# Optimization experiments

Measured on AMD Instinct MI355X. Metric: run time of the kernel, lower is better.

The kernel has to match this reference:

```python
import jax, jax.numpy as jnp
import numpy as np

D_MODEL, D_K, D_V, H = 1024, 128, 128, 8


def setup_inputs() -> dict:
    key = jax.random.key(0)
    ks = jax.random.split(key, 14)
    B, NQ, NK = 8, 1024, 1024
    def lin(kw, out_d, in_d):
        # xavier_uniform weight, zero bias
        lim = jnp.sqrt(6.0 / (in_d + out_d))
        return jax.random.uniform(kw, (out_d, in_d), jnp.float32, -lim, lim)
    return {
        "queries": jax.random.normal(ks[0], (B, NQ, D_MODEL), jnp.float32),
        "keys": jax.random.normal(ks[1], (B, NK, D_MODEL), jnp.float32),
        "values": jax.random.normal(ks[2], (B, NK, D_MODEL), jnp.float32),
        "language_signals": jax.random.normal(ks[3], (B, NQ, D_MODEL), jnp.float32),
        "Wq": lin(ks[4], H * D_K, D_MODEL), "bq": jnp.zeros((H * D_K,), jnp.float32),
        "Wk": lin(ks[5], H * D_K, D_MODEL), "bk": jnp.zeros((H * D_K,), jnp.float32),
        "Wv": lin(ks[6], H * D_V, D_MODEL), "bv": jnp.zeros((H * D_V,), jnp.float32),
        "Ws": lin(ks[7], H * D_K, D_MODEL), "bs": jnp.zeros((H * D_K,), jnp.float32),
        "Wo": lin(ks[8], D_MODEL, H * D_V), "bo": jnp.zeros((D_MODEL,), jnp.float32),
    }


def reference(queries, keys, values, language_signals,
              Wq, bq, Wk, bk, Wv, bv, Ws, bs, Wo, bo):
    b, nq, _ = queries.shape
    nk = keys.shape[1]
    scale = 1.0 / jnp.sqrt(jnp.asarray(D_K, queries.dtype))
    # project and split heads -> (b, h, n, d)
    q = (queries @ Wq.T + bq).reshape(b, nq, H, D_K).transpose(0, 2, 1, 3)
    s = (language_signals @ Ws.T + bs).reshape(b, nq, H, D_K).transpose(0, 2, 1, 3)
    k = (keys @ Wk.T + bk).reshape(b, nk, H, D_K).transpose(0, 2, 1, 3)
    v = (values @ Wv.T + bv).reshape(b, nk, H, D_V).transpose(0, 2, 1, 3)
    attn = jnp.einsum('bhqd,bhkd->bhqk', q, k) * scale           # (b,h,nq,nk)
    lang = jnp.einsum('bhqd,bhqd->bhq', q, s) * scale            # diagonal sentinel score
    combined = jnp.concatenate([attn, lang[..., None]], axis=-1)  # (b,h,nq,nk+1)
    p = jax.nn.softmax(combined, axis=-1)
    # per-query value set is [v; s_i]: split matmul into kv part + sentinel part
    out = jnp.einsum('bhqk,bhkd->bhqd', p[..., :nk], v) + p[..., nk:] * s
    out = out.transpose(0, 2, 1, 3).reshape(b, nq, H * D_V)
    return out @ Wo.T + bo
```

## Files before the change

kernel.cpp:

```cpp
#include <hip/hip_runtime.h>
#include <hip/hip_bf16.h>


typedef __attribute__((ext_vector_type(8))) short s16x8;
typedef __attribute__((ext_vector_type(4))) float f32x4;
typedef __attribute__((ext_vector_type(16))) float f32x16;
typedef __attribute__((ext_vector_type(4))) unsigned int u32x4;

#define DEVI static __device__ __forceinline__

constexpr int BATCH = 8;
constexpr int SEQ   = 1024;
constexpr int NH    = 8;
constexpr int DH    = 128;
constexpr int DM    = 1024;

DEVI short bf16r(float f) {
  __hip_bfloat16 h = __float2bfloat16(f);
  return *reinterpret_cast<short*>(&h);
}
DEVI float bf2f(short s) {
  __hip_bfloat16 h;
  *reinterpret_cast<short*>(&h) = s;
  return __bfloat162float(h);
}
DEVI s16x8 cvt8(const float4& a, const float4& b) {
  s16x8 r;
  r[0] = bf16r(a.x); r[1] = bf16r(a.y); r[2] = bf16r(a.z); r[3] = bf16r(a.w);
  r[4] = bf16r(b.x); r[5] = bf16r(b.y); r[6] = bf16r(b.z); r[7] = bf16r(b.w);
  return r;
}
DEVI unsigned int pack2bf(float a, float b) {
  return (unsigned int)(unsigned short)bf16r(a) |
         ((unsigned int)(unsigned short)bf16r(b) << 16);
}

#define GLOAD16(g, l)                                                        \
  __builtin_amdgcn_global_load_lds(                                          \
      (const __attribute__((address_space(1))) unsigned int*)(g),            \
      (__attribute__((address_space(3))) unsigned int*)(l), 16, 0, 0)

DEVI f32x4 mfma(s16x8 a, s16x8 b, f32x4 c) {
  return __builtin_amdgcn_mfma_f32_16x16x32_bf16(a, b, c, 0, 0, 0);
}
DEVI f32x16 mfma32(s16x8 a, s16x8 b, f32x16 c) {
  return __builtin_amdgcn_mfma_f32_32x32x16_bf16(a, b, c, 0, 0, 0);
}

__global__ __launch_bounds__(256)
void cvt_all(const float* __restrict__ a0, const float* __restrict__ a1,
             const float* __restrict__ a2, const float* __restrict__ a3,
             const float* __restrict__ w0, const float* __restrict__ w1,
             const float* __restrict__ w2, const float* __restrict__ w3,
             const float* __restrict__ w4,
             short* __restrict__ d0, short* __restrict__ d1,
             short* __restrict__ d2, short* __restrict__ d3,
             short* __restrict__ e0, short* __restrict__ e1,
             short* __restrict__ e2, short* __restrict__ e3,
             short* __restrict__ e4) {
  const float* s; short* d; int idx;
  int bid = blockIdx.x;
  if (bid < 16384) {
    int which = bid >> 12; idx = bid & 4095;
    switch (which) {
      case 0: s = a0; d = d0; break;
      case 1: s = a1; d = d1; break;
      case 2: s = a2; d = d2; break;
      default: s = a3; d = d3; break;
    }
  } else {
    int r = bid - 16384;
    int which = r >> 9; idx = r & 511;
    switch (which) {
      case 0: s = w0; d = e0; break;
      case 1: s = w1; d = e1; break;
      case 2: s = w2; d = e2; break;
      case 3: s = w3; d = e3; break;
      default: s = w4; d = e4; break;
    }
  }
  size_t i = ((size_t)idx * 256 + threadIdx.x) * 8;
  float4 a = *(const float4*)(s + i);
  float4 b = *(const float4*)(s + i + 4);
  *(s16x8*)(d + i) = cvt8(a, b);
}

DEVI void gemm_core(const short* __restrict__ A, const short* __restrict__ W,
                    short* Alds, short* Blds, int m0, int n0,
                    f32x4 (&acc)[4][4]) {
  const int tid = threadIdx.x, lane = tid & 63, wid = tid >> 6;
  const int wm = wid >> 1, wn = wid & 1, lr = lane & 15, lg = lane >> 4;
  const int srow = wid * 32 + (lane >> 3);
  const int scb  = (lane & 7) * 16;

  for (int k0 = 0; k0 < DM; k0 += 64) {
    if (k0) __syncthreads();
#pragma unroll
    for (int t = 0; t < 4; t++) {
      int row = srow + t * 8;
      int cbs = scb ^ ((row & 7) << 4);
      GLOAD16((const char*)A + ((size_t)(m0 + row) * DM + k0) * 2 + cbs,
              (char*)Alds + wid * 4096 + t * 1024);
      GLOAD16((const char*)W + ((size_t)(n0 + row) * DM + k0) * 2 + cbs,
              (char*)Blds + wid * 4096 + t * 1024);
    }
    __syncthreads();
#pragma unroll
    for (int kk = 0; kk < 2; kk++) {
      s16x8 af[4], bf[4];
#pragma unroll
      for (int i = 0; i < 4; i++) {
        int row = wm * 64 + i * 16 + lr;
        af[i] = *(const s16x8*)((const char*)Alds + row * 128 +
                                ((kk * 64 + lg * 16) ^ ((row & 7) << 4)));
      }
#pragma unroll
      for (int j = 0; j < 4; j++) {
        int row = wn * 64 + j * 16 + lr;
        bf[j] = *(const s16x8*)((const char*)Blds + row * 128 +
                                ((kk * 64 + lg * 16) ^ ((row & 7) << 4)));
      }
#pragma unroll
      for (int i = 0; i < 4; i++)
#pragma unroll
        for (int j = 0; j < 4; j++)
          acc[i][j] = mfma(af[i], bf[j], acc[i][j]);
    }
  }
}

__global__ __launch_bounds__(256)
void proj_gemm(const short* __restrict__ qa, const short* __restrict__ ka,
               const short* __restrict__ va, const short* __restrict__ sa,
               const short* __restrict__ wq, const short* __restrict__ wk,
               const short* __restrict__ wv, const short* __restrict__ wsn,
               const float* __restrict__ bq, const float* __restrict__ bk,
               const float* __restrict__ bv, const float* __restrict__ bsn,
               short* __restrict__ Qo, short* __restrict__ Ko,
               short* __restrict__ Vo, short* __restrict__ So) {
  __shared__ short Alds[128 * 64];
  __shared__ short Blds[128 * 64];
  const int z = blockIdx.z;
  const short* A; const short* W; const float* bias; short* C;
  switch (z) {
    case 0: A = qa; W = wq;  bias = bq;  C = Qo; break;
    case 1: A = ka; W = wk;  bias = bk;  C = Ko; break;
    case 2: A = va; W = wv;  bias = bv;  C = Vo; break;
    default: A = sa; W = wsn; bias = bsn; C = So; break;
  }
  const int m0 = blockIdx.x * 128, n0 = blockIdx.y * 128;
  f32x4 acc[4][4] = {};
  gemm_core(A, W, Alds, Blds, m0, n0, acc);

  const int lane = threadIdx.x & 63, wid = threadIdx.x >> 6;
  const int wm = wid >> 1, wn = wid & 1, lr = lane & 15, lg = lane >> 4;
#pragma unroll
  for (int i = 0; i < 4; i++) {
#pragma unroll
    for (int r = 0; r < 4; r++) {
      int m = m0 + wm * 64 + i * 16 + lg * 4 + r;
      int bb = m >> 10, sq = m & 1023;
#pragma unroll
      for (int j = 0; j < 4; j++) {
        int n = n0 + wn * 64 + j * 16 + lr;
        float v = acc[i][j][r] + bias[n];
        int hh = n >> 7, d = n & 127;
        if (z == 2)
          C[((size_t)(bb * NH + hh) * DH + d) * SEQ + sq] = bf16r(v);
        else
          C[((size_t)(bb * NH + hh) * SEQ + sq) * DH + d] = bf16r(v);
      }
    }
  }
}

__global__ __launch_bounds__(256)
void out_gemm(const short* __restrict__ A, const short* __restrict__ W,
              const float* __restrict__ bias, float* __restrict__ C) {
  __shared__ short Alds[128 * 64];
  __shared__ short Blds[128 * 64];
  const int bid = blockIdx.x;
  const int wg = (bid & 7) * 64 + (bid >> 3);
  const int m0 = (wg >> 3) * 128, n0 = (wg & 7) * 128;
  f32x4 acc[4][4] = {};
  gemm_core(A, W, Alds, Blds, m0, n0, acc);

  const int lane = threadIdx.x & 63, wid = threadIdx.x >> 6;
  const int wm = wid >> 1, wn = wid & 1, lr = lane & 15, lg = lane >> 4;
#pragma unroll
  for (int i = 0; i < 4; i++)
#pragma unroll
    for (int r = 0; r < 4; r++) {
      int m = m0 + wm * 64 + i * 16 + lg * 4 + r;
#pragma unroll
      for (int j = 0; j < 4; j++) {
        int n = n0 + wn * 64 + j * 16 + lr;
        C[(size_t)m * DM + n] = acc[i][j][r] + bias[n];
      }
    }
}

DEVI void stage_kv(const char* Kg, const char* Vg, int k0n,
                   short* Kd, short* Vd, int tid, int wave) {
  const int krow_l = tid >> 4, kslot = tid & 15;
  const int vrow_l = tid >> 3, vslot = tid & 7;
#pragma unroll
  for (int ln = 0; ln < 2; ln++) {
    int kr = ln * 32 + krow_l;
    int ss = kslot ^ (((kr & 7) << 1) ^ ((kr >> 3) & 3));
    GLOAD16(Kg + (size_t)(k0n + kr) * 256 + ss * 16,
            (char*)Kd + ln * 8192 + wave * 1024);
  }
#pragma unroll
  for (int ln = 0; ln < 2; ln++) {
    int dr = ln * 64 + vrow_l;
    int ss = vslot ^ ((dr & 7) ^ ((dr >> 3) & 3));
    GLOAD16(Vg + (size_t)dr * 2048 + (size_t)k0n * 2 + ss * 16,
            (char*)Vd + ln * 8192 + wave * 1024);
  }
}

__global__ __launch_bounds__(512, 2)
void attn_kernel(const short* __restrict__ Qb, const short* __restrict__ Kb,
                 const short* __restrict__ Vtb, const short* __restrict__ Sb,
                 short* __restrict__ att) {
  __shared__ short Klds[2][64 * 128];
  __shared__ short Vtlds[2][128 * 64];

  const int tid = threadIdx.x, lane = tid & 63, wave = tid >> 6;
  const int l31 = lane & 31, hi = lane >> 5;
  const int bid = blockIdx.x;
  const int logical = (bid & 7) * 32 + (bid >> 3);
  const int hb = logical >> 2, qt = logical & 3;
  const int b = hb >> 3, h = hb & 7;
  const int q0 = qt * 256 + wave * 32;
  const size_t base = (size_t)(b * NH + h) * SEQ * DH;
  const char* Kg = (const char*)(Kb + base);
  const char* Vg = (const char*)(Vtb + base);
  const float scale = 0.08838834764831845f * 1.44269504088896340f;

  s16x8 qf[8];
  {
    const char* qrow = (const char*)(Qb + base) + (size_t)(q0 + l31) * 256 + hi * 16;
#pragma unroll
    for (int kd = 0; kd < 8; kd++) qf[kd] = *(const s16x8*)(qrow + kd * 32);
  }

  float m_run = -INFINITY, l_run = 0.f;
  f32x16 oacc[4] = {};

  const int v4r = ((((lane & 7) << 1) ^ ((lane >> 3) & 3))) << 4;
  const int v3r = (((lane & 7) ^ ((lane >> 3) & 3))) << 4;

  stage_kv(Kg, Vg, 0, Klds[0], Vtlds[0], tid, wave);

  for (int it = 0; it < 16; ++it) {
    const int cur = it & 1;
    __syncthreads();
    if (it < 15)
      stage_kv(Kg, Vg, (it + 1) * 64, Klds[cur ^ 1], Vtlds[cur ^ 1], tid, wave);

    f32x16 st0 = {}, st1 = {};
    const char* Kb0 = (const char*)Klds[cur] + l31 * 256;
    __builtin_amdgcn_s_setprio(1);
#pragma unroll
    for (int kd = 0; kd < 8; kd++) {
      int co = (kd * 32 + hi * 16) ^ v4r;
      s16x8 a0 = *(const s16x8*)(Kb0 + co);
      s16x8 a1 = *(const s16x8*)(Kb0 + 32 * 256 + co);
      st0 = mfma32(a0, qf[kd], st0);
      st1 = mfma32(a1, qf[kd], st1);
    }
    __builtin_amdgcn_s_setprio(0);

    float traw = -INFINITY;
#pragma unroll
    for (int r = 0; r < 16; r++) {
      traw = fmaxf(traw, st0[r]);
      traw = fmaxf(traw, st1[r]);
    }
    traw = fmaxf(traw, __shfl_xor(traw, 32));
    float tmax = traw * scale;
    const bool skip = __all(tmax - m_run <= 8.f);
    float m_new = skip ? m_run : fmaxf(m_run, tmax);
    float psum = 0.f;
    unsigned W0[8], W1[8];
#pragma unroll
    for (int i = 0; i < 8; i++) {
      float p0 = exp2f(fmaf(st0[2 * i],     scale, -m_new));
      float p1 = exp2f(fmaf(st0[2 * i + 1], scale, -m_new));
      float p2 = exp2f(fmaf(st1[2 * i],     scale, -m_new));
      float p3 = exp2f(fmaf(st1[2 * i + 1], scale, -m_new));
      psum += (p0 + p1) + (p2 + p3);
      W0[i] = pack2bf(p0, p1);
      W1[i] = pack2bf(p2, p3);
    }
    psum += __shfl_xor(psum, 32);
    if (skip) {
      l_run += psum;
    } else {
      float fac = exp2f(m_run - m_new);
      l_run = l_run * fac + psum;
      m_run = m_new;
#pragma unroll
      for (int reg = 0; reg < 16; reg++) {
        int qs = (reg & 3) + 8 * (reg >> 2);
        float fr = __shfl(fac, qs + 4 * hi);
#pragma unroll
        for (int dt = 0; dt < 4; dt++) oacc[dt][reg] *= fr;
      }
    }

    s16x8 pa[4];
#pragma unroll
    for (int ks = 0; ks < 4; ks++) {
      const int s4 = (ks & 1) * 4;
      unsigned a0, a1, b0, b1;
      if (ks >> 1) { a0 = W1[s4]; a1 = W1[s4 + 1]; b0 = W1[s4 + 2]; b1 = W1[s4 + 3]; }
      else         { a0 = W0[s4]; a1 = W0[s4 + 1]; b0 = W0[s4 + 2]; b1 = W0[s4 + 3]; }
      unsigned snd0 = hi ? a0 : b0, snd1 = hi ? a1 : b1;
      unsigned rem0 = __shfl_xor(snd0, 32), rem1 = __shfl_xor(snd1, 32);
      unsigned w0 = hi ? rem0 : a0;
      unsigned w1 = hi ? rem1 : a1;
      unsigned w2 = hi ? b0 : rem0;
      unsigned w3 = hi ? b1 : rem1;
      u32x4 t4 = {w0, w1, w2, w3};
      pa[ks] = __builtin_bit_cast(s16x8, t4);
    }

    const char* Vb0 = (const char*)Vtlds[cur] + l31 * 128;
    __builtin_amdgcn_s_setprio(1);
#pragma unroll
    for (int dt = 0; dt < 4; dt++) {
#pragma unroll
      for (int ks = 0; ks < 4; ks++) {
        int co = (ks * 32 + hi * 16) ^ v3r;
        s16x8 bv = *(const s16x8*)(Vb0 + dt * 4096 + co);
        oacc[dt] = mfma32(pa[ks], bv, oacc[dt]);
      }
    }
    __builtin_amdgcn_s_setprio(0);
  }

  s16x8 sf[8];
  {
    const char* srow = (const char*)(Sb + base) + (size_t)(q0 + l31) * 256 + hi * 16;
#pragma unroll
    for (int kd = 0; kd < 8; kd++) sf[kd] = *(const s16x8*)(srow + kd * 32);
  }
  float dot = 0.f;
#pragma unroll
  for (int kd = 0; kd < 8; kd++)
#pragma unroll
    for (int j = 0; j < 8; j++) dot += bf2f(qf[kd][j]) * bf2f(sf[kd][j]);
  dot += __shfl_xor(dot, 32);
  float sc = dot * scale;
  float m_new = fmaxf(m_run, sc);
  float fac = exp2f(m_run - m_new);
  float ps = exp2f(sc - m_new);
  l_run = l_run * fac + ps;
  float inv_l = 1.f / l_run;

#pragma unroll
  for (int reg = 0; reg < 16; reg++) {
    int qs = (reg & 3) + 8 * (reg >> 2) + 4 * hi;
    int qsl = (reg & 3) + 8 * (reg >> 2);
    float fr = __shfl(fac,   qsl + 4 * hi);
    float pr = __shfl(ps,    qsl + 4 * hi);
    float il = __shfl(inv_l, qsl + 4 * hi);
    int qg = q0 + qs;
    const short* Sr = Sb + base + (size_t)qg * DH;
    short* orow = att + ((size_t)b * SEQ + qg) * (NH * DH) + h * DH;
#pragma unroll
    for (int dt = 0; dt < 4; dt++) {
      int d = dt * 32 + l31;
      float v = oacc[dt][reg] * fr + pr * bf2f(Sr[d]);
      orow[d] = bf16r(v * il);
    }
  }
}

extern "C" void kernel_launch(void* const* d_in, const int* in_sizes, int n_in,
                              void* d_out, int out_size, void* d_ws, size_t ws_size,
                              hipStream_t stream) {
  const float* queries = (const float*)d_in[0];
  const float* keys    = (const float*)d_in[1];
  const float* values  = (const float*)d_in[2];
  const float* lang    = (const float*)d_in[3];
  const float* Wq = (const float*)d_in[4];  const float* bq = (const float*)d_in[5];
  const float* Wk = (const float*)d_in[6];  const float* bk = (const float*)d_in[7];
  const float* Wv = (const float*)d_in[8];  const float* bv = (const float*)d_in[9];
  const float* Ws = (const float*)d_in[10]; const float* bs = (const float*)d_in[11];
  const float* Wo = (const float*)d_in[12]; const float* bo = (const float*)d_in[13];
  float* out = (float*)d_out;

  short* ws = (short*)d_ws;
  const size_t NE = (size_t)BATCH * SEQ * DM;
  const size_t WE = (size_t)DM * DM;
  short* qbf = ws;
  short* kbf = qbf + NE;
  short* vbf = kbf + NE;
  short* sbf = vbf + NE;
  short* Qb  = sbf + NE;
  short* Kb  = Qb  + NE;
  short* Vtb = Kb  + NE;
  short* Sb  = Vtb + NE;
  short* wqb = Sb  + NE;
  short* wkb = wqb + WE;
  short* wvb = wkb + WE;
  short* wsb = wvb + WE;
  short* wob = wsb + WE;
  short* att = qbf;

  hipLaunchKernelGGL(cvt_all, dim3(16384 + 2560), dim3(256), 0, stream,
                     queries, keys, values, lang, Wq, Wk, Wv, Ws, Wo,
                     qbf, kbf, vbf, sbf, wqb, wkb, wvb, wsb, wob);

  hipLaunchKernelGGL(proj_gemm, dim3(64, 8, 4), dim3(256), 0, stream,
                     qbf, kbf, vbf, sbf, wqb, wkb, wvb, wsb,
                     bq, bk, bv, bs, Qb, Kb, Vtb, Sb);

  hipLaunchKernelGGL(attn_kernel, dim3(256), dim3(512), 0, stream,
                     Qb, Kb, Vtb, Sb, att);

  hipLaunchKernelGGL(out_gemm, dim3(512), dim3(256), 0, stream,
                     att, wob, bo, out);
}
```

Baseline: 215.6 us.

## Rewrite projection GEMM with 256x256 tiles and double-buffered pipelined loads

Replaces the 128x128-tile projection GEMM with a 512-thread kernel computing 256x256 tiles. It double-buffers LDS and interleaves direct global-to-LDS loads with four MFMA phases per k-step, using barriers and setprio. A swizzled 1D grid is meant to improve L2 reuse. The larger tile cuts global traffic per FLOP and hides load latency, at the cost of heavy LDS use (128KB) and register pressure, plus fewer blocks (512) to fill the CUs.

After: 241.8 us. +12.2%, slower.

```diff
diff --git a/kernel.cpp b/kernel.cpp
--- a/kernel.cpp
+++ b/kernel.cpp
@@ -129,18 +129,27 @@
   }
 }
 
-__global__ __launch_bounds__(256)
-void proj_gemm(const short* __restrict__ qa, const short* __restrict__ ka,
-               const short* __restrict__ va, const short* __restrict__ sa,
-               const short* __restrict__ wq, const short* __restrict__ wk,
-               const short* __restrict__ wv, const short* __restrict__ wsn,
-               const float* __restrict__ bq, const float* __restrict__ bk,
-               const float* __restrict__ bv, const float* __restrict__ bsn,
-               short* __restrict__ Qo, short* __restrict__ Ko,
-               short* __restrict__ Vo, short* __restrict__ So) {
-  __shared__ short Alds[128 * 64];
-  __shared__ short Blds[128 * 64];
-  const int z = blockIdx.z;
+__global__ __launch_bounds__(512, 2)
+void proj_gemm256(const short* __restrict__ qa, const short* __restrict__ ka,
+                  const short* __restrict__ va, const short* __restrict__ sa,
+                  const short* __restrict__ wq, const short* __restrict__ wk,
+                  const short* __restrict__ wv, const short* __restrict__ wsn,
+                  const float* __restrict__ bq, const float* __restrict__ bk,
+                  const float* __restrict__ bv, const float* __restrict__ bsn,
+                  short* __restrict__ Qo, short* __restrict__ Ko,
+                  short* __restrict__ Vo, short* __restrict__ So) {
+  __shared__ short Alds[2][256 * 64];
+  __shared__ short Blds[2][256 * 64];
+
+  const int tid = threadIdx.x, lane = tid & 63, wid = tid >> 6;
+  const int wm = wid >> 2, wn = wid & 3, lr = lane & 15, lg = lane >> 4;
+
+  const int swz = (blockIdx.x & 7) * 64 + (blockIdx.x >> 3);
+  const int z = swz >> 7;
+  const int rem = swz & 127;
+  const int n0 = (rem >> 5) << 8;
+  const int m0 = (rem & 31) << 8;
+
   const short* A; const short* W; const float* bias; short* C;
   switch (z) {
     case 0: A = qa; W = wq;  bias = bq;  C = Qo; break;
@@ -148,22 +157,152 @@
     case 2: A = va; W = wv;  bias = bv;  C = Vo; break;
     default: A = sa; W = wsn; bias = bsn; C = So; break;
   }
-  const int m0 = blockIdx.x * 128, n0 = blockIdx.y * 128;
-  f32x4 acc[4][4] = {};
-  gemm_core(A, W, Alds, Blds, m0, n0, acc);
-
-  const int lane = threadIdx.x & 63, wid = threadIdx.x >> 6;
-  const int wm = wid >> 1, wn = wid & 1, lr = lane & 15, lg = lane >> 4;
-#pragma unroll
-  for (int i = 0; i < 4; i++) {
+  const char* Ag = (const char*)A + (size_t)m0 * 2048;
+  const char* Wg = (const char*)W + (size_t)n0 * 2048;
+
+  const int sR  = wid * 8 + (lane >> 3);
+  const int sCB = (((lane & 7) ^ (lane >> 3)) << 4);
+  const int lgb = lg * 16, rsw = (lr & 7) << 4;
+  const int ko0 = lgb ^ rsw, ko1 = (64 + lgb) ^ rsw;
+
+#define STG(Gb, r0, kb, Lb, off)                                             \
+  GLOAD16((Gb) + (size_t)((r0) + sR) * 2048 + (kb) + sCB,                    \
+          (char*)(Lb) + (off) + wid * 1024)
+
+  {
+    char* pa0 = (char*)Alds[0]; char* pb0 = (char*)Blds[0];
+    char* pa1 = (char*)Alds[1]; char* pb1 = (char*)Blds[1];
+    STG(Ag,   0, 0, pa0, 0);     STG(Ag, 128, 0, pa0, 16384);
+    STG(Ag,  64, 0, pa0, 8192);  STG(Ag, 192, 0, pa0, 24576);
+    STG(Wg,   0, 0, pb0, 0);     STG(Wg,  64, 0, pb0, 8192);
+    STG(Wg, 128, 0, pb0, 16384); STG(Wg, 192, 0, pb0, 24576);
+    STG(Ag,   0, 128, pa1, 0);     STG(Ag, 128, 128, pa1, 16384);
+    STG(Wg,   0, 128, pb1, 0);     STG(Wg,  64, 128, pb1, 8192);
+    STG(Ag,  64, 128, pa1, 8192);  STG(Ag, 192, 128, pa1, 24576);
+  }
+  asm volatile("s_waitcnt vmcnt(6)" ::: "memory");
+  __builtin_amdgcn_s_barrier();
+
+  f32x4 acc[8][4] = {};
+  const int rA0 = wm * 128 + lr;
+  const int rB0 = wn * 64 + lr;
+
+#pragma unroll 2
+  for (int kt = 0; kt < 16; ++kt) {
+    const char* Ab = (const char*)Alds[kt & 1];
+    const char* Bb = (const char*)Blds[kt & 1];
+    char* AbS = (char*)Alds[kt & 1];
+    char* BbS = (char*)Blds[kt & 1];
+    char* BbN = (char*)Blds[(kt + 1) & 1];
+    const int kb1 = (kt + 1) * 128, kb2 = (kt + 2) * 128;
+
+    s16x8 af[8], b0f[4], b1f[4];
+#pragma unroll
+    for (int mf = 0; mf < 4; mf++) {
+      int ro = (rA0 + mf * 16) * 128;
+      af[2 * mf]     = *(const s16x8*)(Ab + ro + ko0);
+      af[2 * mf + 1] = *(const s16x8*)(Ab + ro + ko1);
+    }
+#pragma unroll
+    for (int nf = 0; nf < 2; nf++) {
+      int ro = (rB0 + nf * 16) * 128;
+      b0f[2 * nf]     = *(const s16x8*)(Bb + ro + ko0);
+      b0f[2 * nf + 1] = *(const s16x8*)(Bb + ro + ko1);
+    }
+    if (kt + 1 < 16) {
+      STG(Wg, 128, kb1, BbN, 16384);
+      STG(Wg, 192, kb1, BbN, 24576);
+    }
+    asm volatile("s_waitcnt lgkmcnt(8)" ::: "memory");
+    __builtin_amdgcn_s_barrier();
+    asm volatile("s_waitcnt lgkmcnt(0)" ::: "memory");
+    __builtin_amdgcn_s_setprio(1);
+#pragma unroll
+    for (int mf = 0; mf < 4; mf++)
+#pragma unroll
+      for (int nf = 0; nf < 2; nf++) {
+        acc[mf][nf] = mfma(af[2 * mf],     b0f[2 * nf],     acc[mf][nf]);
+        acc[mf][nf] = mfma(af[2 * mf + 1], b0f[2 * nf + 1], acc[mf][nf]);
+      }
+    __builtin_amdgcn_s_setprio(0);
+    __builtin_amdgcn_s_barrier();
+
+#pragma unroll
+    for (int nf = 0; nf < 2; nf++) {
+      int ro = (rB0 + 32 + nf * 16) * 128;
+      b1f[2 * nf]     = *(const s16x8*)(Bb + ro + ko0);
+      b1f[2 * nf + 1] = *(const s16x8*)(Bb + ro + ko1);
+    }
+    if (kt + 2 < 16) {
+      STG(Ag,   0, kb2, AbS, 0);
+      STG(Ag, 128, kb2, AbS, 16384);
+    }
+    __builtin_amdgcn_s_barrier();
+    asm volatile("s_waitcnt lgkmcnt(0)" ::: "memory");
+    __builtin_amdgcn_s_setprio(1);
+#pragma unroll
+    for (int mf = 0; mf < 4; mf++)
+#pragma unroll
+      for (int nf = 0; nf < 2; nf++) {
+        acc[mf][nf + 2] = mfma(af[2 * mf],     b1f[2 * nf],     acc[mf][nf + 2]);
+        acc[mf][nf + 2] = mfma(af[2 * mf + 1], b1f[2 * nf + 1], acc[mf][nf + 2]);
+      }
+    __builtin_amdgcn_s_setprio(0);
+    __builtin_amdgcn_s_barrier();
+
+#pragma unroll
+    for (int mf = 0; mf < 4; mf++) {
+      int ro = (rA0 + 64 + mf * 16) * 128;
+      af[2 * mf]     = *(const s16x8*)(Ab + ro + ko0);
+      af[2 * mf + 1] = *(const s16x8*)(Ab + ro + ko1);
+    }
+    if (kt + 2 < 16) {
+      STG(Wg,  0, kb2, BbS, 0);
+      STG(Wg, 64, kb2, BbS, 8192);
+    }
+    __builtin_amdgcn_s_barrier();
+    asm volatile("s_waitcnt lgkmcnt(0)" ::: "memory");
+    __builtin_amdgcn_s_setprio(1);
+#pragma unroll
+    for (int mf = 0; mf < 4; mf++)
+#pragma unroll
+      for (int nf = 0; nf < 2; nf++) {
+        acc[mf + 4][nf + 2] = mfma(af[2 * mf],     b1f[2 * nf],     acc[mf + 4][nf + 2]);
+        acc[mf + 4][nf + 2] = mfma(af[2 * mf + 1], b1f[2 * nf + 1], acc[mf + 4][nf + 2]);
+      }
+    __builtin_amdgcn_s_setprio(0);
+    __builtin_amdgcn_s_barrier();
+
+    if (kt + 2 < 16) {
+      STG(Ag,  64, kb2, AbS, 8192);
+      STG(Ag, 192, kb2, AbS, 24576);
+    }
+    __builtin_amdgcn_s_barrier();
+    __builtin_amdgcn_s_setprio(1);
+#pragma unroll
+    for (int mf = 0; mf < 4; mf++)
+#pragma unroll
+      for (int nf = 0; nf < 2; nf++) {
+        acc[mf + 4][nf] = mfma(af[2 * mf],     b0f[2 * nf],     acc[mf + 4][nf]);
+        acc[mf + 4][nf] = mfma(af[2 * mf + 1], b0f[2 * nf + 1], acc[mf + 4][nf]);
+      }
+    __builtin_amdgcn_s_setprio(0);
+    if (kt < 14) asm volatile("s_waitcnt vmcnt(6)" ::: "memory");
+    else         asm volatile("s_waitcnt vmcnt(0)" ::: "memory");
+    __builtin_amdgcn_s_barrier();
+  }
+#undef STG
+
+#pragma unroll
+  for (int mf = 0; mf < 8; mf++) {
 #pragma unroll
     for (int r = 0; r < 4; r++) {
-      int m = m0 + wm * 64 + i * 16 + lg * 4 + r;
+      int m = m0 + wm * 128 + mf * 16 + lg * 4 + r;
       int bb = m >> 10, sq = m & 1023;
 #pragma unroll
-      for (int j = 0; j < 4; j++) {
-        int n = n0 + wn * 64 + j * 16 + lr;
-        float v = acc[i][j][r] + bias[n];
+      for (int nf = 0; nf < 4; nf++) {
+        int n = n0 + wn * 64 + nf * 16 + lr;
+        float v = acc[mf][nf][r] + bias[n];
         int hh = n >> 7, d = n & 127;
         if (z == 2)
           C[((size_t)(bb * NH + hh) * DH + d) * SEQ + sq] = bf16r(v);
@@ -416,7 +555,7 @@
                      queries, keys, values, lang, Wq, Wk, Wv, Ws, Wo,
                      qbf, kbf, vbf, sbf, wqb, wkb, wvb, wsb, wob);
 
-  hipLaunchKernelGGL(proj_gemm, dim3(64, 8, 4), dim3(256), 0, stream,
+  hipLaunchKernelGGL(proj_gemm256, dim3(512), dim3(512), 0, stream,
                      qbf, kbf, vbf, sbf, wqb, wkb, wvb, wsb,
                      bq, bk, bv, bs, Qb, Kb, Vtb, Sb);
 
```
